# Optimization experiments

Hardware: AMD Instinct MI355X
Metric: run time of the kernel (lower is better)

Reference implementation:

```python
import jax, jax.numpy as jnp
import numpy as np

HIDDEN = 1024
STATE = 16
EXPAND = 2
INNER = HIDDEN * EXPAND
BATCH, SEQ = 4, 2048


def setup_inputs() -> dict:
    key = jax.random.key(0)
    ks = jax.random.split(key, 12)
    s = 0.02
    return {
        "x": jax.random.normal(ks[0], (BATCH, SEQ, HIDDEN), jnp.float32),
        "norm_scale": jnp.ones((HIDDEN,), jnp.float32),
        "norm_bias": jnp.zeros((HIDDEN,), jnp.float32),
        "W_in": jax.random.normal(ks[1], (HIDDEN, 2 * INNER), jnp.float32) * s,
        "conv_w": jax.random.normal(ks[2], (INNER, 3), jnp.float32) * 0.3,
        "conv_b": jnp.zeros((INNER,), jnp.float32),
        "W_dt": jax.random.normal(ks[3], (INNER, INNER), jnp.float32) * s,
        "b_dt": jnp.zeros((INNER,), jnp.float32),
        "A_log": jax.random.normal(ks[4], (INNER, STATE), jnp.float32),
        "D_param": jnp.ones((INNER,), jnp.float32),
        "W_B": jax.random.normal(ks[5], (INNER, STATE), jnp.float32) * s,
        "W_C": jax.random.normal(ks[6], (INNER, STATE), jnp.float32) * s,
        "W_out": jax.random.normal(ks[7], (INNER, HIDDEN), jnp.float32) * s,
    }


def reference(x, norm_scale, norm_bias, W_in, conv_w, conv_b, W_dt, b_dt,
              A_log, D_param, W_B, W_C, W_out):
    residual = x
    # LayerNorm (eps = 1e-5, matches nn.LayerNorm default)
    mu = jnp.mean(x, axis=-1, keepdims=True)
    var = jnp.mean(jnp.square(x - mu), axis=-1, keepdims=True)
    xn = (x - mu) * jax.lax.rsqrt(var + 1e-5) * norm_scale + norm_bias

    xz = xn @ W_in                         # [B, L, 2*inner]
    xb, z = jnp.split(xz, 2, axis=-1)      # each [B, L, inner]

    # depthwise conv1d, kernel 3, padding 1 (cross-correlation as in torch)
    xp = jnp.pad(xb, ((0, 0), (1, 1), (0, 0)))
    xb = (conv_w[:, 0] * xp[:, :-2] + conv_w[:, 1] * xp[:, 1:-1]
          + conv_w[:, 2] * xp[:, 2:] + conv_b)
    xb = jax.nn.silu(xb)

    dt = jax.nn.softplus(xb @ W_dt + b_dt)  # [B, L, inner]
    A = -jnp.exp(A_log)                     # [inner, N]
    Bi = xb @ W_B                           # [B, L, N]
    Ci = xb @ W_C                           # [B, L, N]

    def step(h, inp):
        x_t, dt_t, B_t, C_t = inp           # [B,D], [B,D], [B,N], [B,N]
        A_bar = jnp.exp(dt_t[:, :, None] * A)                 # [B, D, N]
        h = A_bar * h + (dt_t * x_t)[:, :, None] * B_t[:, None, :]
        y_t = jnp.einsum('bdn,bn->bd', h, C_t)
        return h, y_t

    h0 = jnp.zeros((x.shape[0], INNER, STATE), x.dtype)
    xs = (jnp.swapaxes(xb, 0, 1), jnp.swapaxes(dt, 0, 1),
          jnp.swapaxes(Bi, 0, 1), jnp.swapaxes(Ci, 0, 1))
    _, y = jax.lax.scan(step, h0, xs)       # y: [L, B, D]
    y = jnp.swapaxes(y, 0, 1)

    y = (y + D_param * xb) * jax.nn.silu(z)
    return residual + y @ W_out
```

## Files before the change

kernel.cpp:

```cpp
#include <hip/hip_runtime.h>
#include <hip/hip_bf16.h>
#include <cstdint>
#include <cstddef>

#define B_DIM 4
#define L_DIM 2048
#define H_DIM 1024
#define D_DIM 2048
#define N_STATE 16
#define TOKENS (B_DIM * L_DIM)
#define CH 16
#define LC (L_DIM / CH)

typedef __bf16 bf16x8 __attribute__((ext_vector_type(8)));
typedef float f32x4 __attribute__((ext_vector_type(4)));

__device__ __forceinline__ float sigmoidf_(float x) { return 1.f / (1.f + __expf(-x)); }
__device__ __forceinline__ float softplusf_(float x) {
  return fmaxf(x, 0.f) + log1pf(__expf(-fabsf(x)));
}
__device__ __forceinline__ void gl_lds16(const void* g, void* l) {
  __builtin_amdgcn_global_load_lds(
      (const __attribute__((address_space(1))) unsigned int*)g,
      (__attribute__((address_space(3))) unsigned int*)l, 16, 0, 0);
}

__global__ __launch_bounds__(256) void ln_kernel(const float* __restrict__ x,
    const float* __restrict__ gamma, const float* __restrict__ beta,
    __hip_bfloat16* __restrict__ out) {
  int row = blockIdx.x;
  int t = threadIdx.x;
  const float* px = x + (size_t)row * H_DIM;
  float4 v = *(const float4*)(px + t * 4);
  float s  = v.x + v.y + v.z + v.w;
  float ss = v.x * v.x + v.y * v.y + v.z * v.z + v.w * v.w;
  for (int off = 32; off > 0; off >>= 1) {
    s  += __shfl_down(s, off);
    ss += __shfl_down(ss, off);
  }
  __shared__ float red[8];
  __shared__ float stats[2];
  int wave = t >> 6, lane = t & 63;
  if (lane == 0) { red[wave] = s; red[4 + wave] = ss; }
  __syncthreads();
  if (t == 0) {
    float S  = red[0] + red[1] + red[2] + red[3];
    float SS = red[4] + red[5] + red[6] + red[7];
    float mu = S / H_DIM;
    float var = SS / H_DIM - mu * mu;
    stats[0] = mu;
    stats[1] = rsqrtf(var + 1e-5f);
  }
  __syncthreads();
  float mu = stats[0], rstd = stats[1];
  float4 g  = *(const float4*)(gamma + t * 4);
  float4 bt = *(const float4*)(beta + t * 4);
  __hip_bfloat16* po = out + (size_t)row * H_DIM + t * 4;
  po[0] = __float2bfloat16((v.x - mu) * rstd * g.x + bt.x);
  po[1] = __float2bfloat16((v.y - mu) * rstd * g.y + bt.y);
  po[2] = __float2bfloat16((v.z - mu) * rstd * g.z + bt.z);
  po[3] = __float2bfloat16((v.w - mu) * rstd * g.w + bt.w);
}

__global__ void transpose_bf16(const float* __restrict__ in,
                               __hip_bfloat16* __restrict__ out, int R, int C) {
  __shared__ float tile[32][33];
  int c0 = blockIdx.x * 32, r0 = blockIdx.y * 32;
  int tx = threadIdx.x, ty = threadIdx.y;
  for (int i = 0; i < 32; i += 8)
    tile[ty + i][tx] = in[(size_t)(r0 + ty + i) * C + c0 + tx];
  __syncthreads();
  for (int i = 0; i < 32; i += 8)
    out[(size_t)(c0 + ty + i) * R + r0 + tx] = __float2bfloat16(tile[tx][ty + i]);
}

#define BM 128
#define BN 128
#define BK 64

__global__ __launch_bounds__(256) void gemm_bf16(
    const __hip_bfloat16* __restrict__ A, const __hip_bfloat16* __restrict__ Bt,
    void* __restrict__ Cout, __hip_bfloat16* __restrict__ Csplit, int nsplit,
    int K, int lda, int ldb, int ldc,
    const float* __restrict__ bias, const float* __restrict__ resid,
    int act, int out_bf16) {
  __shared__ __hip_bfloat16 As[BM * BK];
  __shared__ __hip_bfloat16 Bs[BN * BK];
  int t = threadIdx.x;
  int m0 = blockIdx.y * BM, n0 = blockIdx.x * BN;
  int wave = t >> 6, lane = t & 63;
  int quad = lane >> 4, l16 = lane & 15;
  int wm = (wave >> 1) * 64, wn = (wave & 1) * 64;

  f32x4 acc[4][4] = {};

  int srow  = t >> 3;
  int cslot = t & 7;
  int cdata = cslot ^ (srow & 7);
  const __hip_bfloat16* Ag[4];
  const __hip_bfloat16* Bg[4];
  __hip_bfloat16* Asl[4];
  __hip_bfloat16* Bsl[4];
#pragma unroll
  for (int j = 0; j < 4; ++j) {
    Ag[j]  = A  + (size_t)(m0 + j * 32 + srow) * lda + cdata * 8;
    Bg[j]  = Bt + (size_t)(n0 + j * 32 + srow) * ldb + cdata * 8;
    Asl[j] = &As[(j * 32 + srow) * BK + cslot * 8];
    Bsl[j] = &Bs[(j * 32 + srow) * BK + cslot * 8];
  }

  for (int k0 = 0; k0 < K; k0 += BK) {
    __syncthreads();
#pragma unroll
    for (int j = 0; j < 4; ++j) {
      gl_lds16(Ag[j] + k0, Asl[j]);
      gl_lds16(Bg[j] + k0, Bsl[j]);
    }
    __syncthreads();
#pragma unroll
    for (int s = 0; s < 2; ++s) {
      int cs = ((s * 4 + quad) ^ (l16 & 7)) * 8;
      bf16x8 af[4], bf_[4];
#pragma unroll
      for (int i = 0; i < 4; ++i) {
        af[i]  = *(const bf16x8*)&As[(wm + i * 16 + l16) * BK + cs];
        bf_[i] = *(const bf16x8*)&Bs[(wn + i * 16 + l16) * BK + cs];
      }
#pragma unroll
      for (int i = 0; i < 4; ++i)
#pragma unroll
        for (int j = 0; j < 4; ++j)
          acc[i][j] = __builtin_amdgcn_mfma_f32_16x16x32_bf16(af[i], bf_[j], acc[i][j], 0, 0, 0);
    }
  }

  float* Cf = (float*)Cout;
  __hip_bfloat16* Cb = (__hip_bfloat16*)Cout;
#pragma unroll
  for (int i = 0; i < 4; ++i) {
    int row0 = m0 + wm + i * 16 + quad * 4;
#pragma unroll
    for (int j = 0; j < 4; ++j) {
      int col = n0 + wn + j * 16 + l16;
      f32x4 v = acc[i][j];
      if (bias) {
        float bb = bias[col];
        v[0] += bb; v[1] += bb; v[2] += bb; v[3] += bb;
      }
      if (act == 1) {
        v[0] = softplusf_(v[0]); v[1] = softplusf_(v[1]);
        v[2] = softplusf_(v[2]); v[3] = softplusf_(v[3]);
      }
      __hip_bfloat16* cbp = Cb;
      int ccol = col;
      if (Csplit && col >= nsplit) { cbp = Csplit; ccol = col - nsplit; }
#pragma unroll
      for (int r = 0; r < 4; ++r) {
        float val = v[r];
        if (resid) val += resid[(size_t)(row0 + r) * ldc + col];
        if (out_bf16) cbp[(size_t)(row0 + r) * ldc + ccol] = __float2bfloat16(val);
        else          Cf[(size_t)(row0 + r) * ldc + col] = val;
      }
    }
  }
}

__global__ __launch_bounds__(256) void conv_silu_kernel(const __hip_bfloat16* __restrict__ xb,
    const float* __restrict__ cw, const float* __restrict__ cb,
    __hip_bfloat16* __restrict__ xbc) {
  size_t i2 = (size_t)blockIdx.x * 256 + threadIdx.x;
  int dp = (int)(i2 & (D_DIM / 2 - 1));
  size_t tok = i2 >> 10;
  int l = (int)(tok & (L_DIM - 1));
  int d = dp * 2;
  const __hip_bfloat162* base = (const __hip_bfloat162*)xb + i2;
  __hip_bfloat162 cc = base[0];
  float v0 = cw[d * 3 + 1] * __bfloat162float(cc.x) + cb[d];
  float v1 = cw[d * 3 + 4] * __bfloat162float(cc.y) + cb[d + 1];
  if (l > 0) {
    __hip_bfloat162 pm = base[-(D_DIM / 2)];
    v0 += cw[d * 3 + 0] * __bfloat162float(pm.x);
    v1 += cw[d * 3 + 3] * __bfloat162float(pm.y);
  }
  if (l < L_DIM - 1) {
    __hip_bfloat162 pp = base[D_DIM / 2];
    v0 += cw[d * 3 + 2] * __bfloat162float(pp.x);
    v1 += cw[d * 3 + 5] * __bfloat162float(pp.y);
  }
  v0 = v0 * sigmoidf_(v0);
  v1 = v1 * sigmoidf_(v1);
  __hip_bfloat162 o;
  o.x = __float2bfloat16(v0);
  o.y = __float2bfloat16(v1);
  ((__hip_bfloat162*)xbc)[i2] = o;
}

__global__ __launch_bounds__(256) void bc_kernel(const __hip_bfloat16* __restrict__ xbc,
    const float* __restrict__ WB, const float* __restrict__ WC,
    float* __restrict__ Bi, float* __restrict__ Ci) {
  __shared__ float sA[D_DIM];
  __shared__ float red[8][32];
  int m = blockIdx.x;
  const __hip_bfloat162* a = (const __hip_bfloat162*)(xbc + (size_t)m * D_DIM);
  for (int i = threadIdx.x; i < D_DIM / 2; i += 256) {
    __hip_bfloat162 p = a[i];
    sA[2 * i]     = __bfloat162float(p.x);
    sA[2 * i + 1] = __bfloat162float(p.y);
  }
  __syncthreads();
  int col = threadIdx.x & 31, slice = threadIdx.x >> 5;
  const float* W = (col < 16) ? WB : WC;
  int c = col & 15;
  float s = 0.f;
  int k0 = slice * 256;
  for (int k = 0; k < 256; ++k) s += sA[k0 + k] * W[(k0 + k) * N_STATE + c];
  red[slice][col] = s;
  __syncthreads();
  if (threadIdx.x < 32) {
    float tsum = 0.f;
#pragma unroll
    for (int i = 0; i < 8; ++i) tsum += red[i][col];
    if (col < 16) Bi[(size_t)m * N_STATE + col] = tsum;
    else          Ci[(size_t)m * N_STATE + (col - 16)] = tsum;
  }
}

__global__ __launch_bounds__(256) void scan1_kernel(const float* __restrict__ dt,
    const __hip_bfloat16* __restrict__ xbc, const float* __restrict__ Bi,
    const float* __restrict__ A_log, float* __restrict__ hfin,
    float* __restrict__ dtsum) {
  __shared__ float Bsh[LC * N_STATE];
  int t = threadIdx.x;
  int d = blockIdx.x * 256 + t;
  int c = blockIdx.y, b = blockIdx.z;
  size_t base = (size_t)b * L_DIM + (size_t)c * LC;
  {
    const float4* Bg = (const float4*)(Bi + base * N_STATE);
    float4* Bd = (float4*)Bsh;
    for (int i = t; i < LC * N_STATE / 4; i += 256) Bd[i] = Bg[i];
  }
  float Aneg[N_STATE];
  {
    const float4* Ap = (const float4*)(A_log + (size_t)d * N_STATE);
#pragma unroll
    for (int q = 0; q < 4; ++q) {
      float4 av = Ap[q];
      Aneg[4 * q + 0] = -__expf(av.x);
      Aneg[4 * q + 1] = -__expf(av.y);
      Aneg[4 * q + 2] = -__expf(av.z);
      Aneg[4 * q + 3] = -__expf(av.w);
    }
  }
  __syncthreads();
  const float* dtp = dt + base * D_DIM + d;
  const __hip_bfloat16* xp = xbc + base * D_DIM + d;
  float h[N_STATE];
#pragma unroll
  for (int n = 0; n < N_STATE; ++n) h[n] = 0.f;
  float ds = 0.f;
  float dtv = dtp[0], xv = __bfloat162float(xp[0]);
  for (int i = 0; i < LC; ++i) {
    int ip = (i < LC - 1) ? i + 1 : i;
    float dt2 = dtp[(size_t)ip * D_DIM];
    float x2  = __bfloat162float(xp[(size_t)ip * D_DIM]);
    float dtx = dtv * xv;
    ds += dtv;
    const float4* Brow = (const float4*)&Bsh[i * N_STATE];
#pragma unroll
    for (int q = 0; q < 4; ++q) {
      float4 bv = Brow[q];
      h[4*q+0] = __expf(dtv * Aneg[4*q+0]) * h[4*q+0] + dtx * bv.x;
      h[4*q+1] = __expf(dtv * Aneg[4*q+1]) * h[4*q+1] + dtx * bv.y;
      h[4*q+2] = __expf(dtv * Aneg[4*q+2]) * h[4*q+2] + dtx * bv.z;
      h[4*q+3] = __expf(dtv * Aneg[4*q+3]) * h[4*q+3] + dtx * bv.w;
    }
    dtv = dt2; xv = x2;
  }
  float* ho = hfin + (((size_t)b * CH + c) * D_DIM + d) * N_STATE;
#pragma unroll
  for (int q = 0; q < 4; ++q) {
    float4 v; v.x = h[4*q]; v.y = h[4*q+1]; v.z = h[4*q+2]; v.w = h[4*q+3];
    ((float4*)ho)[q] = v;
  }
  dtsum[((size_t)b * CH + c) * D_DIM + d] = ds;
}

__global__ __launch_bounds__(256) void scan2_kernel(const float* __restrict__ hfin,
    const float* __restrict__ dtsum, const float* __restrict__ A_log,
    float* __restrict__ hstart) {
  int tid = blockIdx.x * 256 + threadIdx.x;
  int n = tid & 15;
  int d = (tid >> 4) & (D_DIM - 1);
  int b = tid >> 15;
  float Aneg = -__expf(A_log[d * N_STATE + n]);
  float run = 0.f;
  for (int c = 0; c < CH; ++c) {
    size_t o = (((size_t)b * CH + c) * D_DIM + d) * N_STATE + n;
    hstart[o] = run;
    run = __expf(Aneg * dtsum[((size_t)b * CH + c) * D_DIM + d]) * run + hfin[o];
  }
}

__global__ __launch_bounds__(256) void scan3_kernel(const float* __restrict__ dt,
    const __hip_bfloat16* __restrict__ xbc, const float* __restrict__ Bi,
    const float* __restrict__ Ci, const float* __restrict__ A_log,
    const float* __restrict__ hstart, const __hip_bfloat16* __restrict__ z,
    const float* __restrict__ Dp, __hip_bfloat16* __restrict__ yo) {
  __shared__ float Bsh[LC * N_STATE];
  __shared__ float Csh[LC * N_STATE];
  int t = threadIdx.x;
  int d = blockIdx.x * 256 + t;
  int c = blockIdx.y, b = blockIdx.z;
  size_t base = (size_t)b * L_DIM + (size_t)c * LC;
  {
    const float4* Bg = (const float4*)(Bi + base * N_STATE);
    const float4* Cg = (const float4*)(Ci + base * N_STATE);
    float4* Bd = (float4*)Bsh;
    float4* Cd = (float4*)Csh;
    for (int i = t; i < LC * N_STATE / 4; i += 256) { Bd[i] = Bg[i]; Cd[i] = Cg[i]; }
  }
  float Aneg[N_STATE];
  {
    const float4* Ap = (const float4*)(A_log + (size_t)d * N_STATE);
#pragma unroll
    for (int q = 0; q < 4; ++q) {
      float4 av = Ap[q];
      Aneg[4 * q + 0] = -__expf(av.x);
      Aneg[4 * q + 1] = -__expf(av.y);
      Aneg[4 * q + 2] = -__expf(av.z);
      Aneg[4 * q + 3] = -__expf(av.w);
    }
  }
  float h[N_STATE];
  {
    const float4* hs = (const float4*)(hstart + (((size_t)b * CH + c) * D_DIM + d) * N_STATE);
#pragma unroll
    for (int q = 0; q < 4; ++q) {
      float4 v = hs[q];
      h[4*q] = v.x; h[4*q+1] = v.y; h[4*q+2] = v.z; h[4*q+3] = v.w;
    }
  }
  float Dv = Dp[d];
  __syncthreads();
  const float* dtp = dt + base * D_DIM + d;
  const __hip_bfloat16* xp = xbc + base * D_DIM + d;
  const __hip_bfloat16* zp = z + base * D_DIM + d;
  __hip_bfloat16* yp = yo + base * D_DIM + d;
  float dtv = dtp[0], xv = __bfloat162float(xp[0]);
  float zv = __bfloat162float(zp[0]);
  for (int i = 0; i < LC; ++i) {
    int ip = (i < LC - 1) ? i + 1 : i;
    float dt2 = dtp[(size_t)ip * D_DIM];
    float x2  = __bfloat162float(xp[(size_t)ip * D_DIM]);
    float z2  = __bfloat162float(zp[(size_t)ip * D_DIM]);
    float dtx = dtv * xv;
    const float4* Brow = (const float4*)&Bsh[i * N_STATE];
    const float4* Crow = (const float4*)&Csh[i * N_STATE];
    float yv = 0.f;
#pragma unroll
    for (int q = 0; q < 4; ++q) {
      float4 bv = Brow[q];
      float4 cv = Crow[q];
      h[4*q+0] = __expf(dtv * Aneg[4*q+0]) * h[4*q+0] + dtx * bv.x;
      h[4*q+1] = __expf(dtv * Aneg[4*q+1]) * h[4*q+1] + dtx * bv.y;
      h[4*q+2] = __expf(dtv * Aneg[4*q+2]) * h[4*q+2] + dtx * bv.z;
      h[4*q+3] = __expf(dtv * Aneg[4*q+3]) * h[4*q+3] + dtx * bv.w;
      yv += h[4*q+0] * cv.x + h[4*q+1] * cv.y + h[4*q+2] * cv.z + h[4*q+3] * cv.w;
    }
    float g = zv * sigmoidf_(zv);
    yp[(size_t)i * D_DIM] = __float2bfloat16((yv + Dv * xv) * g);
    dtv = dt2; xv = x2; zv = z2;
  }
}

extern "C" void kernel_launch(void* const* d_in, const int* in_sizes, int n_in,
                              void* d_out, int out_size, void* d_ws, size_t ws_size,
                              hipStream_t stream) {
  const float* x          = (const float*)d_in[0];
  const float* norm_scale = (const float*)d_in[1];
  const float* norm_bias  = (const float*)d_in[2];
  const float* W_in       = (const float*)d_in[3];
  const float* conv_w     = (const float*)d_in[4];
  const float* conv_b     = (const float*)d_in[5];
  const float* W_dt       = (const float*)d_in[6];
  const float* b_dt       = (const float*)d_in[7];
  const float* A_log      = (const float*)d_in[8];
  const float* D_param    = (const float*)d_in[9];
  const float* W_B        = (const float*)d_in[10];
  const float* W_C        = (const float*)d_in[11];
  const float* W_out      = (const float*)d_in[12];
  float* out = (float*)d_out;

  const size_t MB = 1024 * 1024;
  const size_t NEEDED = 193 * MB;
  if (ws_size < NEEDED) return;

  char* ws = (char*)d_ws;
  __hip_bfloat16* xn     = (__hip_bfloat16*)(ws);
  __hip_bfloat16* W_outT = (__hip_bfloat16*)(ws);
  float*          hfin   = (float*)(ws + 4 * MB);
  float*          dtsum  = (float*)(ws + 12 * MB);
  __hip_bfloat16* xb     = (__hip_bfloat16*)(ws + 16 * MB);
  __hip_bfloat16* ybf    = (__hip_bfloat16*)(ws + 16 * MB);
  __hip_bfloat16* z      = (__hip_bfloat16*)(ws + 48 * MB);
  __hip_bfloat16* xbc    = (__hip_bfloat16*)(ws + 80 * MB);
  float*          dtY    = (float*)(ws + 112 * MB);
  float*          Bi     = (float*)(ws + 176 * MB);
  float*          Ci     = Bi + (size_t)TOKENS * N_STATE;
  __hip_bfloat16* W_inT  = (__hip_bfloat16*)(ws + 177 * MB);
  float*          hstart = (float*)(ws + 177 * MB);
  __hip_bfloat16* W_dtT  = (__hip_bfloat16*)(ws + 185 * MB);

  dim3 tb(32, 8);
  transpose_bf16<<<dim3(4096 / 32, 1024 / 32), tb, 0, stream>>>(W_in, W_inT, 1024, 4096);
  transpose_bf16<<<dim3(2048 / 32, 2048 / 32), tb, 0, stream>>>(W_dt, W_dtT, 2048, 2048);
  ln_kernel<<<TOKENS, 256, 0, stream>>>(x, norm_scale, norm_bias, xn);
  gemm_bf16<<<dim3(2 * D_DIM / BN, TOKENS / BM), 256, 0, stream>>>(
      xn, W_inT, xb, z, D_DIM, H_DIM, H_DIM, H_DIM, D_DIM,
      nullptr, nullptr, 0, 1);
  transpose_bf16<<<dim3(1024 / 32, 2048 / 32), tb, 0, stream>>>(W_out, W_outT, 2048, 1024);
  conv_silu_kernel<<<(TOKENS * D_DIM / 2) / 256, 256, 0, stream>>>(xb, conv_w, conv_b, xbc);
  gemm_bf16<<<dim3(D_DIM / BN, TOKENS / BM), 256, 0, stream>>>(
      xbc, W_dtT, dtY, nullptr, 1 << 30, D_DIM, D_DIM, D_DIM, D_DIM,
      b_dt, nullptr, 1, 0);
  bc_kernel<<<TOKENS, 256, 0, stream>>>(xbc, W_B, W_C, Bi, Ci);
  scan1_kernel<<<dim3(D_DIM / 256, CH, B_DIM), 256, 0, stream>>>(
      dtY, xbc, Bi, A_log, hfin, dtsum);
  scan2_kernel<<<(B_DIM * D_DIM * N_STATE) / 256, 256, 0, stream>>>(
      hfin, dtsum, A_log, hstart);
  scan3_kernel<<<dim3(D_DIM / 256, CH, B_DIM), 256, 0, stream>>>(
      dtY, xbc, Bi, Ci, A_log, hstart, z, D_param, ybf);
  gemm_bf16<<<dim3(H_DIM / BN, TOKENS / BM), 256, 0, stream>>>(
      ybf, W_outT, out, nullptr, 1 << 30, D_DIM, D_DIM, D_DIM, H_DIM,
      nullptr, x, 0, 0);
}
```

Measured before the change: 681.0 us.

## Fuse B/C projections into dt GEMM, store dt as bf16, swizzle GEMM tiles

Appends W_B and W_C as 32 extra columns to the transposed W_dt, padded to 2176 columns, so the dt GEMM also produces Bi/Ci into a 128-stride fp32 buffer. This removes the separate bc_kernel and its scalar reduction over xbc. dt is now written as bf16, which halves the scan kernels' dt traffic at some cost in precision. GEMM blocks are remapped to a grouped ordering of 8 M-tiles for better L2 reuse, and the extra N tile adds wasted compute on padded columns.

```diff
diff --git a/kernel.cpp b/kernel.cpp
--- a/kernel.cpp
+++ b/kernel.cpp
@@ -11,6 +11,7 @@
 #define TOKENS (B_DIM * L_DIM)
 #define CH 16
 #define LC (L_DIM / CH)
+#define NEXT 2176
 
 typedef __bf16 bf16x8 __attribute__((ext_vector_type(8)));
 typedef float f32x4 __attribute__((ext_vector_type(4)));
@@ -74,20 +75,38 @@
     out[(size_t)(c0 + ty + i) * R + r0 + tx] = __float2bfloat16(tile[tx][ty + i]);
 }
 
+__global__ __launch_bounds__(256) void wbc_transpose(const float* __restrict__ WB,
+    const float* __restrict__ WC, __hip_bfloat16* __restrict__ Wext) {
+  int tid = blockIdx.x * 256 + threadIdx.x;
+  int c = tid & 31;
+  int k0 = (tid >> 5) * 16;
+  const float* W = (c < 16) ? WB : WC;
+  int cc = c & 15;
+  __hip_bfloat16* o = Wext + (size_t)(2048 + c) * D_DIM + k0;
+  for (int kk = 0; kk < 16; ++kk)
+    o[kk] = __float2bfloat16(W[(size_t)(k0 + kk) * N_STATE + cc]);
+}
+
 #define BM 128
 #define BN 128
 #define BK 64
 
 __global__ __launch_bounds__(256) void gemm_bf16(
     const __hip_bfloat16* __restrict__ A, const __hip_bfloat16* __restrict__ Bt,
-    void* __restrict__ Cout, __hip_bfloat16* __restrict__ Csplit, int nsplit,
-    int K, int lda, int ldb, int ldc,
-    const float* __restrict__ bias, const float* __restrict__ resid,
-    int act, int out_bf16) {
+    void* __restrict__ C0, void* __restrict__ C1, int nsplit,
+    int K, int lda, int ldb, int ldc, int gx,
+    const float* __restrict__ bias, int nbias,
+    const float* __restrict__ resid, int act, int mode) {
   __shared__ __hip_bfloat16 As[BM * BK];
   __shared__ __hip_bfloat16 Bs[BN * BK];
   int t = threadIdx.x;
-  int m0 = blockIdx.y * BM, n0 = blockIdx.x * BN;
+  int bid = blockIdx.x;
+  int nsup = gx << 3;
+  int super = bid / nsup;
+  int rem = bid - super * nsup;
+  int m0 = (super * 8 + (rem & 7)) * BM;
+  int n0 = (rem >> 3) * BN;
+
   int wave = t >> 6, lane = t & 63;
   int quad = lane >> 4, l16 = lane & 15;
   int wm = (wave >> 1) * 64, wn = (wave & 1) * 64;
@@ -134,8 +153,6 @@
     }
   }
 
-  float* Cf = (float*)Cout;
-  __hip_bfloat16* Cb = (__hip_bfloat16*)Cout;
 #pragma unroll
   for (int i = 0; i < 4; ++i) {
     int row0 = m0 + wm + i * 16 + quad * 4;
@@ -143,23 +160,29 @@
     for (int j = 0; j < 4; ++j) {
       int col = n0 + wn + j * 16 + l16;
       f32x4 v = acc[i][j];
-      if (bias) {
+      bool mainc = (col < nsplit);
+      if (bias && col < nbias) {
         float bb = bias[col];
         v[0] += bb; v[1] += bb; v[2] += bb; v[3] += bb;
       }
-      if (act == 1) {
+      if (act == 1 && (mode != 2 || mainc)) {
         v[0] = softplusf_(v[0]); v[1] = softplusf_(v[1]);
         v[2] = softplusf_(v[2]); v[3] = softplusf_(v[3]);
       }
-      __hip_bfloat16* cbp = Cb;
-      int ccol = col;
-      if (Csplit && col >= nsplit) { cbp = Csplit; ccol = col - nsplit; }
 #pragma unroll
       for (int r = 0; r < 4; ++r) {
         float val = v[r];
-        if (resid) val += resid[(size_t)(row0 + r) * ldc + col];
-        if (out_bf16) cbp[(size_t)(row0 + r) * ldc + ccol] = __float2bfloat16(val);
-        else          Cf[(size_t)(row0 + r) * ldc + col] = val;
+        size_t row = row0 + r;
+        if (mode == 0) {
+          if (resid) val += resid[row * ldc + col];
+          ((float*)C0)[row * ldc + col] = val;
+        } else if (mode == 1) {
+          if (mainc) ((__hip_bfloat16*)C0)[row * ldc + col] = __float2bfloat16(val);
+          else       ((__hip_bfloat16*)C1)[row * ldc + (col - nsplit)] = __float2bfloat16(val);
+        } else {
+          if (mainc) ((__hip_bfloat16*)C0)[row * ldc + col] = __float2bfloat16(val);
+          else       ((float*)C1)[row * 128 + (col - nsplit)] = val;
+        }
       }
     }
   }
@@ -195,38 +218,8 @@
   ((__hip_bfloat162*)xbc)[i2] = o;
 }
 
-__global__ __launch_bounds__(256) void bc_kernel(const __hip_bfloat16* __restrict__ xbc,
-    const float* __restrict__ WB, const float* __restrict__ WC,
-    float* __restrict__ Bi, float* __restrict__ Ci) {
-  __shared__ float sA[D_DIM];
-  __shared__ float red[8][32];
-  int m = blockIdx.x;
-  const __hip_bfloat162* a = (const __hip_bfloat162*)(xbc + (size_t)m * D_DIM);
-  for (int i = threadIdx.x; i < D_DIM / 2; i += 256) {
-    __hip_bfloat162 p = a[i];
-    sA[2 * i]     = __bfloat162float(p.x);
-    sA[2 * i + 1] = __bfloat162float(p.y);
-  }
-  __syncthreads();
-  int col = threadIdx.x & 31, slice = threadIdx.x >> 5;
-  const float* W = (col < 16) ? WB : WC;
-  int c = col & 15;
-  float s = 0.f;
-  int k0 = slice * 256;
-  for (int k = 0; k < 256; ++k) s += sA[k0 + k] * W[(k0 + k) * N_STATE + c];
-  red[slice][col] = s;
-  __syncthreads();
-  if (threadIdx.x < 32) {
-    float tsum = 0.f;
-#pragma unroll
-    for (int i = 0; i < 8; ++i) tsum += red[i][col];
-    if (col < 16) Bi[(size_t)m * N_STATE + col] = tsum;
-    else          Ci[(size_t)m * N_STATE + (col - 16)] = tsum;
-  }
-}
-
-__global__ __launch_bounds__(256) void scan1_kernel(const float* __restrict__ dt,
-    const __hip_bfloat16* __restrict__ xbc, const float* __restrict__ Bi,
+__global__ __launch_bounds__(256) void scan1_kernel(const __hip_bfloat16* __restrict__ dt,
+    const __hip_bfloat16* __restrict__ xbc, const float* __restrict__ BiCi,
     const float* __restrict__ A_log, float* __restrict__ hfin,
     float* __restrict__ dtsum) {
   __shared__ float Bsh[LC * N_STATE];
@@ -234,10 +227,9 @@
   int d = blockIdx.x * 256 + t;
   int c = blockIdx.y, b = blockIdx.z;
   size_t base = (size_t)b * L_DIM + (size_t)c * LC;
-  {
-    const float4* Bg = (const float4*)(Bi + base * N_STATE);
-    float4* Bd = (float4*)Bsh;
-    for (int i = t; i < LC * N_STATE / 4; i += 256) Bd[i] = Bg[i];
+  for (int idx = t; idx < LC * 4; idx += 256) {
+    int row = idx >> 2, q = idx & 3;
+    ((float4*)Bsh)[row * 4 + q] = *(const float4*)&BiCi[(base + row) * 128 + q * 4];
   }
   float Aneg[N_STATE];
   {
@@ -252,16 +244,16 @@
     }
   }
   __syncthreads();
-  const float* dtp = dt + base * D_DIM + d;
+  const __hip_bfloat16* dtp = dt + base * D_DIM + d;
   const __hip_bfloat16* xp = xbc + base * D_DIM + d;
   float h[N_STATE];
 #pragma unroll
   for (int n = 0; n < N_STATE; ++n) h[n] = 0.f;
   float ds = 0.f;
-  float dtv = dtp[0], xv = __bfloat162float(xp[0]);
+  float dtv = __bfloat162float(dtp[0]), xv = __bfloat162float(xp[0]);
   for (int i = 0; i < LC; ++i) {
     int ip = (i < LC - 1) ? i + 1 : i;
-    float dt2 = dtp[(size_t)ip * D_DIM];
+    float dt2 = __bfloat162float(dtp[(size_t)ip * D_DIM]);
     float x2  = __bfloat162float(xp[(size_t)ip * D_DIM]);
     float dtx = dtv * xv;
     ds += dtv;
@@ -301,9 +293,9 @@
   }
 }
 
-__global__ __launch_bounds__(256) void scan3_kernel(const float* __restrict__ dt,
-    const __hip_bfloat16* __restrict__ xbc, const float* __restrict__ Bi,
-    const float* __restrict__ Ci, const float* __restrict__ A_log,
+__global__ __launch_bounds__(256) void scan3_kernel(const __hip_bfloat16* __restrict__ dt,
+    const __hip_bfloat16* __restrict__ xbc, const float* __restrict__ BiCi,
+    const float* __restrict__ A_log,
     const float* __restrict__ hstart, const __hip_bfloat16* __restrict__ z,
     const float* __restrict__ Dp, __hip_bfloat16* __restrict__ yo) {
   __shared__ float Bsh[LC * N_STATE];
@@ -312,12 +304,10 @@
   int d = blockIdx.x * 256 + t;
   int c = blockIdx.y, b = blockIdx.z;
   size_t base = (size_t)b * L_DIM + (size_t)c * LC;
-  {
-    const float4* Bg = (const float4*)(Bi + base * N_STATE);
-    const float4* Cg = (const float4*)(Ci + base * N_STATE);
-    float4* Bd = (float4*)Bsh;
-    float4* Cd = (float4*)Csh;
-    for (int i = t; i < LC * N_STATE / 4; i += 256) { Bd[i] = Bg[i]; Cd[i] = Cg[i]; }
+  for (int idx = t; idx < LC * 4; idx += 256) {
+    int row = idx >> 2, q = idx & 3;
+    ((float4*)Bsh)[row * 4 + q] = *(const float4*)&BiCi[(base + row) * 128 + q * 4];
+    ((float4*)Csh)[row * 4 + q] = *(const float4*)&BiCi[(base + row) * 128 + 16 + q * 4];
   }
   float Aneg[N_STATE];
   {
@@ -342,15 +332,15 @@
   }
   float Dv = Dp[d];
   __syncthreads();
-  const float* dtp = dt + base * D_DIM + d;
+  const __hip_bfloat16* dtp = dt + base * D_DIM + d;
   const __hip_bfloat16* xp = xbc + base * D_DIM + d;
   const __hip_bfloat16* zp = z + base * D_DIM + d;
   __hip_bfloat16* yp = yo + base * D_DIM + d;
-  float dtv = dtp[0], xv = __bfloat162float(xp[0]);
+  float dtv = __bfloat162float(dtp[0]), xv = __bfloat162float(xp[0]);
   float zv = __bfloat162float(zp[0]);
   for (int i = 0; i < LC; ++i) {
     int ip = (i < LC - 1) ? i + 1 : i;
-    float dt2 = dtp[(size_t)ip * D_DIM];
+    float dt2 = __bfloat162float(dtp[(size_t)ip * D_DIM]);
     float x2  = __bfloat162float(xp[(size_t)ip * D_DIM]);
     float z2  = __bfloat162float(zp[(size_t)ip * D_DIM]);
     float dtx = dtv * xv;
@@ -404,33 +394,32 @@
   __hip_bfloat16* ybf    = (__hip_bfloat16*)(ws + 16 * MB);
   __hip_bfloat16* z      = (__hip_bfloat16*)(ws + 48 * MB);
   __hip_bfloat16* xbc    = (__hip_bfloat16*)(ws + 80 * MB);
-  float*          dtY    = (float*)(ws + 112 * MB);
-  float*          Bi     = (float*)(ws + 176 * MB);
-  float*          Ci     = Bi + (size_t)TOKENS * N_STATE;
+  __hip_bfloat16* dtY    = (__hip_bfloat16*)(ws + 112 * MB);
+  float*          BiCi   = (float*)(ws + 144 * MB);
+  __hip_bfloat16* W_ext  = (__hip_bfloat16*)(ws + 148 * MB);
   __hip_bfloat16* W_inT  = (__hip_bfloat16*)(ws + 177 * MB);
   float*          hstart = (float*)(ws + 177 * MB);
-  __hip_bfloat16* W_dtT  = (__hip_bfloat16*)(ws + 185 * MB);
 
   dim3 tb(32, 8);
   transpose_bf16<<<dim3(4096 / 32, 1024 / 32), tb, 0, stream>>>(W_in, W_inT, 1024, 4096);
-  transpose_bf16<<<dim3(2048 / 32, 2048 / 32), tb, 0, stream>>>(W_dt, W_dtT, 2048, 2048);
+  transpose_bf16<<<dim3(2048 / 32, 2048 / 32), tb, 0, stream>>>(W_dt, W_ext, 2048, 2048);
+  wbc_transpose<<<16, 256, 0, stream>>>(W_B, W_C, W_ext);
   ln_kernel<<<TOKENS, 256, 0, stream>>>(x, norm_scale, norm_bias, xn);
-  gemm_bf16<<<dim3(2 * D_DIM / BN, TOKENS / BM), 256, 0, stream>>>(
-      xn, W_inT, xb, z, D_DIM, H_DIM, H_DIM, H_DIM, D_DIM,
-      nullptr, nullptr, 0, 1);
+  gemm_bf16<<<(4096 / BN) * (TOKENS / BM), 256, 0, stream>>>(
+      xn, W_inT, xb, z, D_DIM, H_DIM, H_DIM, H_DIM, D_DIM, 4096 / BN,
+      nullptr, 0, nullptr, 0, 1);
   transpose_bf16<<<dim3(1024 / 32, 2048 / 32), tb, 0, stream>>>(W_out, W_outT, 2048, 1024);
   conv_silu_kernel<<<(TOKENS * D_DIM / 2) / 256, 256, 0, stream>>>(xb, conv_w, conv_b, xbc);
-  gemm_bf16<<<dim3(D_DIM / BN, TOKENS / BM), 256, 0, stream>>>(
-      xbc, W_dtT, dtY, nullptr, 1 << 30, D_DIM, D_DIM, D_DIM, D_DIM,
-      b_dt, nullptr, 1, 0);
-  bc_kernel<<<TOKENS, 256, 0, stream>>>(xbc, W_B, W_C, Bi, Ci);
+  gemm_bf16<<<(NEXT / BN) * (TOKENS / BM), 256, 0, stream>>>(
+      xbc, W_ext, dtY, BiCi, D_DIM, D_DIM, D_DIM, D_DIM, D_DIM, NEXT / BN,
+      b_dt, D_DIM, nullptr, 1, 2);
   scan1_kernel<<<dim3(D_DIM / 256, CH, B_DIM), 256, 0, stream>>>(
-      dtY, xbc, Bi, A_log, hfin, dtsum);
+      dtY, xbc, BiCi, A_log, hfin, dtsum);
   scan2_kernel<<<(B_DIM * D_DIM * N_STATE) / 256, 256, 0, stream>>>(
       hfin, dtsum, A_log, hstart);
   scan3_kernel<<<dim3(D_DIM / 256, CH, B_DIM), 256, 0, stream>>>(
-      dtY, xbc, Bi, Ci, A_log, hstart, z, D_param, ybf);
-  gemm_bf16<<<dim3(H_DIM / BN, TOKENS / BM), 256, 0, stream>>>(
-      ybf, W_outT, out, nullptr, 1 << 30, D_DIM, D_DIM, D_DIM, H_DIM,
-      nullptr, x, 0, 0);
-}
+      dtY, xbc, BiCi, A_log, hstart, z, D_param, ybf);
+  gemm_bf16<<<(H_DIM / BN) * (TOKENS / BM), 256, 0, stream>>>(
+      ybf, W_outT, out, nullptr, 1 << 30, D_DIM, D_DIM, D_DIM, H_DIM, H_DIM / BN,
+      nullptr, 0, x, 0, 0);
+}
```

New measurement: 678.3 us. Within noise of the previous version (-0.4%).
